# Kernel tuning notes

Hardware: AMD Instinct MI355X
Metric: run time of the kernel (lower is better)

## Reference

```python
import jax, jax.numpy as jnp
import numpy as np

F_SIZE = 1024
N_HEADS = 16
HEAD = F_SIZE // N_HEADS
EPS = 1e-5


def setup_inputs() -> dict:
    key = jax.random.key(0)
    ks = jax.random.split(key, 8)
    B, N, F = 4, 1024, F_SIZE
    in_feats = jax.random.normal(ks[0], (B, N, F), dtype=jnp.float32)
    pos_feats = jax.random.normal(ks[1], (B, N, F), dtype=jnp.float32)
    # parameters (torch Linear convention: W [out, in], y = x @ W.T + b)
    xav = lambda k, o, i: jax.random.uniform(k, (o, i), jnp.float32, -1.0, 1.0) * np.sqrt(6.0 / (o + i))
    ln_g = jnp.ones((F,), jnp.float32)
    ln_b = jnp.zeros((F,), jnp.float32)
    w_qk = xav(ks[2], 2 * F, F)
    b_qk = jnp.zeros((2 * F,), jnp.float32)
    w_v = xav(ks[3], F, F)
    b_v = jnp.zeros((F,), jnp.float32)
    w_o = xav(ks[4], F, F)
    b_o = jnp.zeros((F,), jnp.float32)
    return {"in_feats": in_feats, "pos_feats": pos_feats, "ln_g": ln_g, "ln_b": ln_b,
            "w_qk": w_qk, "b_qk": b_qk, "w_v": w_v, "b_v": b_v, "w_o": w_o, "b_o": b_o}


def reference(in_feats, pos_feats, ln_g, ln_b, w_qk, b_qk, w_v, b_v, w_o, b_o):
    B, N, F = in_feats.shape
    H, D = N_HEADS, HEAD
    # LayerNorm (biased variance, eps=1e-5 as torch default)
    mu = jnp.mean(in_feats, axis=-1, keepdims=True)
    var = jnp.mean(jnp.square(in_feats - mu), axis=-1, keepdims=True)
    norm = (in_feats - mu) * jax.lax.rsqrt(var + EPS) * ln_g + ln_b
    pos_norm = norm + pos_feats
    # QK projection on pos-added features, V projection on norm features
    qk = pos_norm @ w_qk.T + b_qk                      # [B,N,2F]
    q = qk[..., :F].reshape(B, N, H, D)
    k = qk[..., F:].reshape(B, N, H, D)
    v = (norm @ w_v.T + b_v).reshape(B, N, H, D)
    scale = float(D) ** -0.5
    scores = jnp.einsum('bnhd,bmhd->bhnm', q, k) * scale
    attn = jax.nn.softmax(scores, axis=-1)
    wv = jnp.einsum('bhnm,bmhd->bnhd', attn, v).reshape(B, N, F)
    delta = wv @ w_o.T + b_o
    return in_feats + delta
```

## Files before the change

### kernel.cpp

```cpp
#include <hip/hip_runtime.h>
#include <hip/hip_bf16.h>
#include <stdint.h>

#define FDIM 1024
#define NHEADS 16
#define HDIM 64
#define BATCH 4
#define SEQ 1024
#define MROWS (BATCH*SEQ)

typedef short bf16x8 __attribute__((ext_vector_type(8)));
typedef float f32x4 __attribute__((ext_vector_type(4)));

__device__ inline unsigned short f2bf(float f){
  union { float f; uint32_t u; } v; v.f = f;
  uint32_t u = v.u;
  uint32_t r = (u + 0x7fffu + ((u >> 16) & 1u)) >> 16;
  return (unsigned short)r;
}

__device__ inline void gld_lds16(const void* g, void* l){
  __builtin_amdgcn_global_load_lds((const __attribute__((address_space(1))) uint32_t*)g,
                                   (__attribute__((address_space(3))) uint32_t*)l, 16, 0, 0);
}

__device__ inline bf16x8 ldsw(const unsigned short* base, int row, int colgrp){
  return *(const bf16x8*)&base[row*64 + (((colgrp) ^ (row&7))<<3)];
}

template<int N>
__device__ inline float dppRor(float x){
  int r = __builtin_amdgcn_update_dpp(0, __float_as_int(x), 0x120|N, 0xF, 0xF, true);
  return __int_as_float(r);
}
__device__ inline float rowMax16(float x){
  x = fmaxf(x, dppRor<1>(x)); x = fmaxf(x, dppRor<2>(x));
  x = fmaxf(x, dppRor<4>(x)); x = fmaxf(x, dppRor<8>(x));
  return x;
}
__device__ inline float rowSum16(float x){
  x += dppRor<1>(x); x += dppRor<2>(x); x += dppRor<4>(x); x += dppRor<8>(x);
  return x;
}

__global__ __launch_bounds__(256) void cvt_all(const float* __restrict__ wqk,
                                               const float* __restrict__ wv,
                                               const float* __restrict__ wo,
                                               unsigned short* __restrict__ oqk,
                                               unsigned short* __restrict__ ov,
                                               unsigned short* __restrict__ oo){
  int i = blockIdx.x*256 + threadIdx.x;
  const float* src; unsigned short* dst; int j;
  if (i < 524288)      { src = wqk; dst = oqk; j = i; }
  else if (i < 786432) { src = wv;  dst = ov;  j = i - 524288; }
  else                 { src = wo;  dst = oo;  j = i - 786432; }
  float4 v = ((const float4*)src)[j];
  ushort4 o; o.x=f2bf(v.x); o.y=f2bf(v.y); o.z=f2bf(v.z); o.w=f2bf(v.w);
  ((ushort4*)dst)[j] = o;
}

__global__ __launch_bounds__(256) void ln_posadd(const float* __restrict__ x,
                                                 const float* __restrict__ pos,
                                                 const float* __restrict__ g,
                                                 const float* __restrict__ be,
                                                 unsigned short* __restrict__ normb,
                                                 unsigned short* __restrict__ posnb){
  int row = blockIdx.x, t = threadIdx.x;
  float4 v = ((const float4*)(x + (size_t)row*FDIM))[t];
  float s  = v.x+v.y+v.z+v.w;
  float sq = v.x*v.x+v.y*v.y+v.z*v.z+v.w*v.w;
  #pragma unroll
  for (int off=32; off>=1; off>>=1){ s += __shfl_down(s,off); sq += __shfl_down(sq,off); }
  __shared__ float red[8];
  int w=t>>6, lane=t&63;
  if (!lane){ red[w]=s; red[4+w]=sq; }
  __syncthreads();
  s  = red[0]+red[1]+red[2]+red[3];
  sq = red[4]+red[5]+red[6]+red[7];
  float mu  = s*(1.0f/FDIM);
  float var = sq*(1.0f/FDIM) - mu*mu;
  float rs  = rsqrtf(var + 1e-5f);
  float4 gg=((const float4*)g)[t], bb=((const float4*)be)[t];
  float4 pp=((const float4*)(pos + (size_t)row*FDIM))[t];
  float n0=(v.x-mu)*rs*gg.x+bb.x, n1=(v.y-mu)*rs*gg.y+bb.y;
  float n2=(v.z-mu)*rs*gg.z+bb.z, n3=(v.w-mu)*rs*gg.w+bb.w;
  ushort4 nb; nb.x=f2bf(n0); nb.y=f2bf(n1); nb.z=f2bf(n2); nb.w=f2bf(n3);
  ushort4 pb; pb.x=f2bf(n0+pp.x); pb.y=f2bf(n1+pp.y); pb.z=f2bf(n2+pp.z); pb.w=f2bf(n3+pp.w);
  ((ushort4*)(normb+(size_t)row*FDIM))[t]=nb;
  ((ushort4*)(posnb+(size_t)row*FDIM))[t]=pb;
}

template<int MODE>
__global__ __launch_bounds__(256) void gemm_bt(const unsigned short* __restrict__ A,
                                               const unsigned short* __restrict__ Bw,
                                               const float* __restrict__ bias,
                                               const float* __restrict__ resid,
                                               void* __restrict__ Cout,
                                               int M, int Nout, int K){
  __shared__ unsigned short Als[128*32];
  __shared__ unsigned short Bls[128*32];
  int t = threadIdx.x, w = t>>6, lane = t&63;
  int m0 = blockIdx.x*128, n0 = blockIdx.y*128;
  int wm = (w>>1)*64, wn = (w&1)*64;
  int lrow = lane&15, lk = (lane>>4)*8, rg = lane>>4;
  f32x4 acc[4][4] = {};
  for (int k0=0; k0<K; k0+=32){
    #pragma unroll
    for (int i=0;i<2;i++){
      int c = t + i*256;
      gld_lds16(A  + (size_t)(m0 + (c>>2))*K + k0 + (c&3)*8, Als + c*8);
      gld_lds16(Bw + (size_t)(n0 + (c>>2))*K + k0 + (c&3)*8, Bls + c*8);
    }
    __syncthreads();
    bf16x8 a[4], b[4];
    #pragma unroll
    for (int i=0;i<4;i++){
      a[i] = *(const bf16x8*)&Als[(wm + i*16 + lrow)*32 + lk];
      b[i] = *(const bf16x8*)&Bls[(wn + i*16 + lrow)*32 + lk];
    }
    #pragma unroll
    for (int mi=0;mi<4;mi++)
      #pragma unroll
      for (int ni=0;ni<4;ni++)
        acc[mi][ni] = __builtin_amdgcn_mfma_f32_16x16x32_bf16(a[mi], b[ni], acc[mi][ni], 0,0,0);
    __syncthreads();
  }
  #pragma unroll
  for (int mi=0;mi<4;mi++){
    #pragma unroll
    for (int ni=0;ni<4;ni++){
      int n = n0 + wn + ni*16 + lrow;
      float bs = (MODE==2) ? 0.f : bias[n];
      #pragma unroll
      for (int r=0;r<4;r++){
        int m = m0 + wm + mi*16 + rg*4 + r;
        float vv = acc[mi][ni][r] + ((MODE==2) ? bias[m] : bs);
        size_t idx = (size_t)m*Nout + n;
        if (MODE==1) ((float*)Cout)[idx] = vv + resid[idx];
        else         ((unsigned short*)Cout)[idx] = f2bf(vv);
      }
    }
  }
}

__global__ __launch_bounds__(256) void attn(const unsigned short* __restrict__ qk,
                                            const unsigned short* __restrict__ vt,
                                            unsigned short* __restrict__ wvbuf){
  __shared__ unsigned short Qls[64*64];
  __shared__ unsigned short Kls[2][64*64];
  __shared__ unsigned short Vtls[2][64*64];
  __shared__ unsigned short Pls[64*64];
  int t=threadIdx.x, w=t>>6, lane=t&63;
  int lrow=lane&15, lcg=lane>>4, rg=lane>>4;
  int bid = blockIdx.x;
  int wgid = (bid&7)*128 + (bid>>3);
  int q0 = (wgid&15)*64, h = (wgid>>4)&15, b = wgid>>8;
  const size_t qs = 2*FDIM;

  #pragma unroll
  for (int i=0;i<2;i++){
    int c=t+i*256, row=c>>3, cg=(c&7)^(row&7);
    gld_lds16(qk + (size_t)(b*SEQ + q0 + row)*qs + h*HDIM + cg*8, Qls + c*8);
    gld_lds16(qk + (size_t)(b*SEQ + row)*qs + FDIM + h*HDIM + cg*8, Kls[0] + c*8);
    gld_lds16(vt + (size_t)(h*HDIM + row)*MROWS + b*SEQ + cg*8, Vtls[0] + c*8);
  }
  f32x4 o[4] = {};
  float m_run[4], l_run[4];
  #pragma unroll
  for (int r=0;r<4;r++){ m_run[r]=-1e30f; l_run[r]=0.f; }
  __syncthreads();
  bf16x8 qa[2];
  qa[0] = ldsw(Qls, w*16+lrow, 0*4 + lcg);
  qa[1] = ldsw(Qls, w*16+lrow, 1*4 + lcg);

  const float SCL = 0.125f * 1.44269504f;
  int cur = 0;

  for (int kt=0; kt<16; ++kt){
    if (kt < 15){
      int key1 = (kt+1)*64;
      #pragma unroll
      for (int i=0;i<2;i++){
        int c=t+i*256, row=c>>3, cg=(c&7)^(row&7);
        gld_lds16(qk + (size_t)(b*SEQ + key1 + row)*qs + FDIM + h*HDIM + cg*8, Kls[cur^1] + c*8);
        gld_lds16(vt + (size_t)(h*HDIM + row)*MROWS + b*SEQ + key1 + cg*8, Vtls[cur^1] + c*8);
      }
    }
    f32x4 s[4] = {};
    #pragma unroll
    for (int kf=0; kf<2; kf++){
      #pragma unroll
      for (int ni=0;ni<4;ni++){
        bf16x8 kb = ldsw(Kls[cur], ni*16+lrow, kf*4 + lcg);
        s[ni] = __builtin_amdgcn_mfma_f32_16x16x32_bf16(qa[kf], kb, s[ni], 0,0,0);
      }
    }
    #pragma unroll
    for (int r=0;r<4;r++){
      float tm = fmaxf(fmaxf(s[0][r],s[1][r]), fmaxf(s[2][r],s[3][r])) * SCL;
      tm = rowMax16(tm);
      float mn = fmaxf(m_run[r], tm);
      float sc = exp2f(m_run[r] - mn);
      float p[4]; float ts = 0.f;
      #pragma unroll
      for (int ni=0;ni<4;ni++){ p[ni] = exp2f(s[ni][r]*SCL - mn); ts += p[ni]; }
      ts = rowSum16(ts);
      l_run[r] = l_run[r]*sc + ts;
      m_run[r] = mn;
      #pragma unroll
      for (int nd=0;nd<4;nd++) o[nd][r] *= sc;
      int pr = w*16 + rg*4 + r;
      #pragma unroll
      for (int ni=0;ni<4;ni++)
        Pls[pr*64 + (((ni*2 + (lrow>>3)) ^ (pr&7))<<3) + (lrow&7)] = f2bf(p[ni]);
    }
    #pragma unroll
    for (int kf=0; kf<2; kf++){
      bf16x8 pa = ldsw(Pls, w*16+lrow, kf*4 + lcg);
      #pragma unroll
      for (int nd=0;nd<4;nd++){
        bf16x8 vb = ldsw(Vtls[cur], nd*16+lrow, kf*4 + lcg);
        o[nd] = __builtin_amdgcn_mfma_f32_16x16x32_bf16(pa, vb, o[nd], 0,0,0);
      }
    }
    __syncthreads();
    cur ^= 1;
  }
  #pragma unroll
  for (int nd=0; nd<4; nd++){
    #pragma unroll
    for (int r=0;r<4;r++){
      float val = o[nd][r] / l_run[r];
      wvbuf[(size_t)(b*SEQ + q0 + w*16 + rg*4 + r)*FDIM + h*HDIM + nd*16 + lrow] = f2bf(val);
    }
  }
}

extern "C" void kernel_launch(void* const* d_in, const int* in_sizes, int n_in,
                              void* d_out, int out_size, void* d_ws, size_t ws_size,
                              hipStream_t stream) {
  const float* in_feats = (const float*)d_in[0];
  const float* pos      = (const float*)d_in[1];
  const float* ln_g     = (const float*)d_in[2];
  const float* ln_b     = (const float*)d_in[3];
  const float* w_qk     = (const float*)d_in[4];
  const float* b_qk     = (const float*)d_in[5];
  const float* w_v      = (const float*)d_in[6];
  const float* b_v      = (const float*)d_in[7];
  const float* w_o      = (const float*)d_in[8];
  const float* b_o      = (const float*)d_in[9];
  float* out = (float*)d_out;

  char* ws = (char*)d_ws;
  unsigned short* norm_b = (unsigned short*)(ws + 0);
  unsigned short* posn_b = (unsigned short*)(ws + (8u<<20));
  unsigned short* wqk_b  = (unsigned short*)(ws + (16u<<20));
  unsigned short* wv_b   = (unsigned short*)(ws + (20u<<20));
  unsigned short* wo_b   = (unsigned short*)(ws + (22u<<20));
  unsigned short* qk_buf = (unsigned short*)(ws + (24u<<20));
  unsigned short* vt_buf = (unsigned short*)(ws + (40u<<20));
  unsigned short* wv_out = norm_b;

  cvt_all<<<4096, 256, 0, stream>>>(w_qk, w_v, w_o, wqk_b, wv_b, wo_b);
  ln_posadd<<<MROWS, 256, 0, stream>>>(in_feats, pos, ln_g, ln_b, norm_b, posn_b);
  gemm_bt<0><<<dim3(MROWS/128, 2048/128), 256, 0, stream>>>(posn_b, wqk_b, b_qk, nullptr,
                                                            qk_buf, MROWS, 2048, FDIM);
  gemm_bt<2><<<dim3(FDIM/128, MROWS/128), 256, 0, stream>>>(wv_b, norm_b, b_v, nullptr,
                                                            vt_buf, FDIM, MROWS, FDIM);
  attn<<<dim3(SEQ/64 * NHEADS * BATCH), 256, 0, stream>>>(qk_buf, vt_buf, wv_out);
  gemm_bt<1><<<dim3(MROWS/128, 1024/128), 256, 0, stream>>>(wv_out, wo_b, b_o, in_feats,
                                                            out, MROWS, 1024, FDIM);
}
```

Measured before the change: 257.2 us.

## Load attention K/V fragments directly from global memory and prescale Q in projection

The attention kernel stops staging Q, K and V tiles through double-buffered LDS with async global-to-LDS loads. Each wave now reads its MFMA operand fragments straight from global memory, relying on cache reuse, which drops the per-tile barrier. The softmax scale times log2(e) is folded into the Q half of the QK projection epilogue through a new GEMM mode, and occupancy is hinted with launch_bounds(256,4). This trades LDS traffic and barriers for many more scattered global loads that are redundant across the four waves and exposed in latency without prefetch, and rounding Q to bf16 after scaling slightly changes numerics.

Measured after the change: 305.2 us. 1.19x slower.

```diff
diff --git a/kernel.cpp b/kernel.cpp
--- a/kernel.cpp
+++ b/kernel.cpp
@@ -90,6 +90,7 @@
   ((ushort4*)(posnb+(size_t)row*FDIM))[t]=pb;
 }
 
+#define QSCL 0.1803368801111204f
 template<int MODE>
 __global__ __launch_bounds__(256) void gemm_bt(const unsigned short* __restrict__ A,
                                                const unsigned short* __restrict__ Bw,
@@ -131,10 +132,12 @@
     for (int ni=0;ni<4;ni++){
       int n = n0 + wn + ni*16 + lrow;
       float bs = (MODE==2) ? 0.f : bias[n];
+      float scl = (MODE==3 && n < FDIM) ? QSCL : 1.0f;
       #pragma unroll
       for (int r=0;r<4;r++){
         int m = m0 + wm + mi*16 + rg*4 + r;
         float vv = acc[mi][ni][r] + ((MODE==2) ? bias[m] : bs);
+        if (MODE==3) vv *= scl;
         size_t idx = (size_t)m*Nout + n;
         if (MODE==1) ((float*)Cout)[idx] = vv + resid[idx];
         else         ((unsigned short*)Cout)[idx] = f2bf(vv);
@@ -143,12 +146,9 @@
   }
 }
 
-__global__ __launch_bounds__(256) void attn(const unsigned short* __restrict__ qk,
-                                            const unsigned short* __restrict__ vt,
-                                            unsigned short* __restrict__ wvbuf){
-  __shared__ unsigned short Qls[64*64];
-  __shared__ unsigned short Kls[2][64*64];
-  __shared__ unsigned short Vtls[2][64*64];
+__global__ __launch_bounds__(256, 4) void attn(const unsigned short* __restrict__ qk,
+                                               const unsigned short* __restrict__ vt,
+                                               unsigned short* __restrict__ wvbuf){
   __shared__ unsigned short Pls[64*64];
   int t=threadIdx.x, w=t>>6, lane=t&63;
   int lrow=lane&15, lcg=lane>>4, rg=lane>>4;
@@ -157,53 +157,36 @@
   int q0 = (wgid&15)*64, h = (wgid>>4)&15, b = wgid>>8;
   const size_t qs = 2*FDIM;
 
-  #pragma unroll
-  for (int i=0;i<2;i++){
-    int c=t+i*256, row=c>>3, cg=(c&7)^(row&7);
-    gld_lds16(qk + (size_t)(b*SEQ + q0 + row)*qs + h*HDIM + cg*8, Qls + c*8);
-    gld_lds16(qk + (size_t)(b*SEQ + row)*qs + FDIM + h*HDIM + cg*8, Kls[0] + c*8);
-    gld_lds16(vt + (size_t)(h*HDIM + row)*MROWS + b*SEQ + cg*8, Vtls[0] + c*8);
-  }
+  const unsigned short* qrow = qk + (size_t)(b*SEQ + q0 + w*16 + lrow)*qs + h*HDIM;
+  bf16x8 qa0 = *(const bf16x8*)(qrow + lcg*8);
+  bf16x8 qa1 = *(const bf16x8*)(qrow + 32 + lcg*8);
+
+  const unsigned short* kbase = qk + (size_t)(b*SEQ + lrow)*qs + FDIM + h*HDIM + lcg*8;
+  const unsigned short* vbase = vt + (size_t)(h*HDIM + lrow)*MROWS + b*SEQ + lcg*8;
+
   f32x4 o[4] = {};
   float m_run[4], l_run[4];
   #pragma unroll
   for (int r=0;r<4;r++){ m_run[r]=-1e30f; l_run[r]=0.f; }
-  __syncthreads();
-  bf16x8 qa[2];
-  qa[0] = ldsw(Qls, w*16+lrow, 0*4 + lcg);
-  qa[1] = ldsw(Qls, w*16+lrow, 1*4 + lcg);
-
-  const float SCL = 0.125f * 1.44269504f;
-  int cur = 0;
 
   for (int kt=0; kt<16; ++kt){
-    if (kt < 15){
-      int key1 = (kt+1)*64;
-      #pragma unroll
-      for (int i=0;i<2;i++){
-        int c=t+i*256, row=c>>3, cg=(c&7)^(row&7);
-        gld_lds16(qk + (size_t)(b*SEQ + key1 + row)*qs + FDIM + h*HDIM + cg*8, Kls[cur^1] + c*8);
-        gld_lds16(vt + (size_t)(h*HDIM + row)*MROWS + b*SEQ + key1 + cg*8, Vtls[cur^1] + c*8);
-      }
-    }
     f32x4 s[4] = {};
     #pragma unroll
-    for (int kf=0; kf<2; kf++){
-      #pragma unroll
-      for (int ni=0;ni<4;ni++){
-        bf16x8 kb = ldsw(Kls[cur], ni*16+lrow, kf*4 + lcg);
-        s[ni] = __builtin_amdgcn_mfma_f32_16x16x32_bf16(qa[kf], kb, s[ni], 0,0,0);
-      }
+    for (int ni=0;ni<4;ni++){
+      bf16x8 kb0 = *(const bf16x8*)(kbase + (size_t)(kt*64 + ni*16)*qs);
+      bf16x8 kb1 = *(const bf16x8*)(kbase + (size_t)(kt*64 + ni*16)*qs + 32);
+      s[ni] = __builtin_amdgcn_mfma_f32_16x16x32_bf16(qa0, kb0, s[ni], 0,0,0);
+      s[ni] = __builtin_amdgcn_mfma_f32_16x16x32_bf16(qa1, kb1, s[ni], 0,0,0);
     }
     #pragma unroll
     for (int r=0;r<4;r++){
-      float tm = fmaxf(fmaxf(s[0][r],s[1][r]), fmaxf(s[2][r],s[3][r])) * SCL;
+      float tm = fmaxf(fmaxf(s[0][r],s[1][r]), fmaxf(s[2][r],s[3][r]));
       tm = rowMax16(tm);
       float mn = fmaxf(m_run[r], tm);
       float sc = exp2f(m_run[r] - mn);
       float p[4]; float ts = 0.f;
       #pragma unroll
-      for (int ni=0;ni<4;ni++){ p[ni] = exp2f(s[ni][r]*SCL - mn); ts += p[ni]; }
+      for (int ni=0;ni<4;ni++){ p[ni] = exp2f(s[ni][r] - mn); ts += p[ni]; }
       ts = rowSum16(ts);
       l_run[r] = l_run[r]*sc + ts;
       m_run[r] = mn;
@@ -219,12 +202,10 @@
       bf16x8 pa = ldsw(Pls, w*16+lrow, kf*4 + lcg);
       #pragma unroll
       for (int nd=0;nd<4;nd++){
-        bf16x8 vb = ldsw(Vtls[cur], nd*16+lrow, kf*4 + lcg);
+        bf16x8 vb = *(const bf16x8*)(vbase + (size_t)(nd*16)*MROWS + kt*64 + kf*32);
         o[nd] = __builtin_amdgcn_mfma_f32_16x16x32_bf16(pa, vb, o[nd], 0,0,0);
       }
     }
-    __syncthreads();
-    cur ^= 1;
   }
   #pragma unroll
   for (int nd=0; nd<4; nd++){
@@ -263,7 +244,7 @@
 
   cvt_all<<<4096, 256, 0, stream>>>(w_qk, w_v, w_o, wqk_b, wv_b, wo_b);
   ln_posadd<<<MROWS, 256, 0, stream>>>(in_feats, pos, ln_g, ln_b, norm_b, posn_b);
-  gemm_bt<0><<<dim3(MROWS/128, 2048/128), 256, 0, stream>>>(posn_b, wqk_b, b_qk, nullptr,
+  gemm_bt<3><<<dim3(MROWS/128, 2048/128), 256, 0, stream>>>(posn_b, wqk_b, b_qk, nullptr,
                                                             qk_buf, MROWS, 2048, FDIM);
   gemm_bt<2><<<dim3(FDIM/128, MROWS/128), 256, 0, stream>>>(wv_b, norm_b, b_v, nullptr,
                                                             vt_buf, FDIM, MROWS, FDIM);
```
